# Kernel optimization log

Hardware: AMD Instinct MI355X
Metric: run time of the kernel (lower is better)

## Reference

```python
import jax, jax.numpy as jnp
import numpy as np

B, T, N = 8, 128, 64
K, d = 8, 64
D = K * d  # 512
NEG = -32767.0  # -2**15 + 1, as in the torch module


def _xavier(key, shape):
    fan_out, fan_in = shape
    limit = float(np.sqrt(6.0 / (fan_in + fan_out)))
    return jax.random.uniform(key, shape, jnp.float32, -limit, limit)


def setup_inputs() -> dict:
    key = jax.random.key(0)
    ks = jax.random.split(key, 6)
    X = jax.random.normal(ks[0], (B, T, N, D), jnp.float32)
    STE = jax.random.normal(ks[1], (B, T, N, 2 * D), jnp.float32)
    Wq = _xavier(ks[2], (D, 3 * D))
    Wk = _xavier(ks[3], (D, 3 * D))
    Wv = _xavier(ks[4], (D, 3 * D))
    Wo = _xavier(ks[5], (D, D))
    bq = jnp.zeros((D,), jnp.float32)
    bk = jnp.zeros((D,), jnp.float32)
    bv = jnp.zeros((D,), jnp.float32)
    bo = jnp.zeros((D,), jnp.float32)
    return {"X": X, "STE": STE, "Wq": Wq, "bq": bq, "Wk": Wk, "bk": bk,
            "Wv": Wv, "bv": bv, "Wo": Wo, "bo": bo}


def _fc(H, W, b):
    # 1x1 conv over channel dim == linear on last axis, then ReLU
    return jax.nn.relu(jnp.einsum('btnc,oc->btno', H, W) + b)


def _split_heads(x):
    # [B,T,N,D] -> [K,B,N,T,d]; torch splits last dim into K chunks of d and
    # stacks them along the batch dim (head-major), then permutes (0,2,1,3).
    return x.reshape(B, T, N, K, d).transpose(3, 0, 2, 1, 4)


def reference(X, STE, Wq, bq, Wk, bk, Wv, bv, Wo, bo):
    H = jnp.concatenate([X, STE], axis=-1)  # [B,T,N,3D]
    q = _split_heads(_fc(H, Wq, bq))  # [K,B,N,T,d]
    k = _split_heads(_fc(H, Wk, bk))
    v = _split_heads(_fc(H, Wv, bv))
    att = jnp.einsum('kbntd,kbnsd->kbnts', q, k) / jnp.sqrt(jnp.float32(d))
    causal = jnp.tril(jnp.ones((T, T), bool))  # [T,T]
    att = jnp.where(causal, att, NEG)
    att = jax.nn.softmax(att, axis=-1)
    out = jnp.einsum('kbnts,kbnsd->kbntd', att, v)  # [K,B,N,T,d]
    out = out.transpose(1, 3, 2, 0, 4).reshape(B, T, N, D)  # heads back to channels
    return jax.nn.relu(jnp.einsum('btnc,oc->btno', out, Wo) + bo)
```

## Files before the change

### kernel.cpp

```cpp
#include <hip/hip_runtime.h>
#include <hip/hip_bf16.h>


typedef __attribute__((ext_vector_type(8))) short short8;
typedef __attribute__((ext_vector_type(8))) _Float16 half8;
typedef __attribute__((ext_vector_type(4))) float floatx4;
typedef __attribute__((ext_vector_type(4))) unsigned int uintx4;

static __device__ __forceinline__ ushort f2b(float f) {
  __hip_bfloat16 h = __float2bfloat16(f);
  return __builtin_bit_cast(ushort, h);
}
static __device__ __forceinline__ ushort f2h(float f) {
  _Float16 h = (_Float16)f;
  return __builtin_bit_cast(ushort, h);
}
static __device__ __forceinline__ float blo(unsigned int w) {
  return __builtin_bit_cast(float, w << 16);
}
static __device__ __forceinline__ float bhi(unsigned int w) {
  return __builtin_bit_cast(float, w & 0xffff0000u);
}
static __device__ __forceinline__ uintx4 cvt8(const float* __restrict__ p) {
  const floatx4 f0 = *(const floatx4*)(p);
  const floatx4 f1 = *(const floatx4*)(p + 4);
  uintx4 r;
  r[0] = (unsigned int)f2b(f0[0]) | ((unsigned int)f2b(f0[1]) << 16);
  r[1] = (unsigned int)f2b(f0[2]) | ((unsigned int)f2b(f0[3]) << 16);
  r[2] = (unsigned int)f2b(f1[0]) | ((unsigned int)f2b(f1[1]) << 16);
  r[3] = (unsigned int)f2b(f1[2]) | ((unsigned int)f2b(f1[3]) << 16);
  return r;
}
static __device__ __forceinline__ void gld_lds16(const ushort* g, ushort* l) {
  __builtin_amdgcn_global_load_lds(
      (const __attribute__((address_space(1))) void*)g,
      (__attribute__((address_space(3))) void*)l, 16, 0, 0);
}

__global__ __launch_bounds__(256)
void cvt_bf16_pass(const float* __restrict__ X, const float* __restrict__ STE,
                   const float* __restrict__ Wq, const float* __restrict__ Wk,
                   const float* __restrict__ Wv, const float* __restrict__ Wo,
                   ushort* __restrict__ H, ushort* __restrict__ Wb,
                   ushort* __restrict__ Wob)
{
  const int stride = gridDim.x * blockDim.x;
  for (int c = blockIdx.x * blockDim.x + threadIdx.x; c < 12910592; c += stride) {
    const float* src; ushort* dst;
    if (c < 4194304) {
      const int m = c >> 6, col = (c & 63) << 3;
      src = X + ((size_t)c << 3);
      dst = H + (size_t)m * 1536 + col;
    } else if (c < 12582912) {
      const int c2 = c - 4194304;
      const int m = c2 >> 7, col = (c2 & 127) << 3;
      src = STE + ((size_t)c2 << 3);
      dst = H + (size_t)m * 1536 + 512 + col;
    } else if (c < 12877824) {
      const int c3 = c - 12582912;
      const int w = c3 / 98304;
      const int r = c3 - w * 98304;
      const float* Ws = (w == 0) ? Wq : (w == 1) ? Wk : Wv;
      src = Ws + ((size_t)r << 3);
      dst = Wb + ((size_t)c3 << 3);
    } else {
      const int c4 = c - 12877824;
      src = Wo + ((size_t)c4 << 3);
      dst = Wob + ((size_t)c4 << 3);
    }
    *(uintx4*)dst = cvt8(src);
  }
}

template<int KDIM, bool TRIPLE, bool OUT_F32>
__global__ __launch_bounds__(256, 2)
void gemm_bf16_async(const ushort* __restrict__ A, const ushort* __restrict__ Wall,
                     const float* __restrict__ b0, const float* __restrict__ b1,
                     const float* __restrict__ b2, void* __restrict__ Cv, int ldc)
{
  __shared__ ushort As[128 * 64];
  __shared__ ushort Bs[128 * 64];

  const int tn = blockIdx.x, tm = blockIdx.y;
  const int tid = threadIdx.x;
  const int wave = tid >> 6, lane = tid & 63;
  const int quad = lane >> 4, lid = lane & 15;
  const int wm = wave >> 1, wn = wave & 1;

  const ushort* W; const float* bias; int nbase, cbase;
  if (TRIPLE) {
    const int seg = tn >> 2;
    W = Wall + (size_t)seg * 512 * 1536;
    bias = (seg == 0) ? b0 : (seg == 1) ? b1 : b2;
    nbase = (tn & 3) * 128;
    cbase = seg * 512;
  } else { W = Wall; bias = b0; nbase = tn * 128; cbase = 0; }

  const int rloc = lane >> 3, sphys = lane & 7;

  floatx4 acc[4][4];
#pragma unroll
  for (int i = 0; i < 4; i++)
#pragma unroll
    for (int j = 0; j < 4; j++) acc[i][j] = (floatx4){0.f, 0.f, 0.f, 0.f};

  const char* AsB = (const char*)As;
  const char* BsB = (const char*)Bs;

  for (int kt = 0; kt < KDIM / 64; ++kt) {
#pragma unroll
    for (int i = 0; i < 4; i++) {
      const int row = (wave * 4 + i) * 8 + rloc;
      const int slog = sphys ^ (row & 7);
      const int k0 = kt * 64 + slog * 8;
      gld_lds16(A + (size_t)(tm * 128 + row) * KDIM + k0, As + (wave * 4 + i) * 512);
      gld_lds16(W + (size_t)(nbase + row) * KDIM + k0,    Bs + (wave * 4 + i) * 512);
    }
    __syncthreads();
#pragma unroll
    for (int ks = 0; ks < 2; ++ks) {
      short8 af[4], bfr[4];
#pragma unroll
      for (int t = 0; t < 4; t++) {
        const int ar = wm * 64 + t * 16 + lid;
        const int br = wn * 64 + t * 16 + lid;
        af[t]  = *(const short8*)(AsB + ar * 128 + (((ks * 4 + quad) ^ (ar & 7)) << 4));
        bfr[t] = *(const short8*)(BsB + br * 128 + (((ks * 4 + quad) ^ (br & 7)) << 4));
      }
#pragma unroll
      for (int i = 0; i < 4; i++)
#pragma unroll
        for (int j = 0; j < 4; j++)
          acc[i][j] = __builtin_amdgcn_mfma_f32_16x16x32_bf16(af[i], bfr[j], acc[i][j], 0, 0, 0);
    }
    __syncthreads();
  }

#pragma unroll
  for (int j = 0; j < 4; j++) {
    const int ncol = nbase + wn * 64 + j * 16 + lid;
    const float bv = bias[ncol];
    const int cg = cbase + ncol;
#pragma unroll
    for (int i = 0; i < 4; i++) {
      const int mrow = tm * 128 + wm * 64 + i * 16 + quad * 4;
#pragma unroll
      for (int r = 0; r < 4; r++) {
        float v = acc[i][j][r] + bv;
        v = v > 0.f ? v : 0.f;
        if (OUT_F32) ((float*)Cv)[(size_t)(mrow + r) * ldc + cg] = v;
        else         ((ushort*)Cv)[(size_t)(mrow + r) * ldc + cg] = f2b(v);
      }
    }
  }
}

__global__ __launch_bounds__(256, 2)
void attn_mfma(const ushort* __restrict__ qkv, ushort* __restrict__ outb)
{
  __shared__ ushort Ks[128 * 64];
  __shared__ ushort Vt[64 * 128];
  __shared__ ushort Ps[128 * 128];

  const int bx = blockIdx.x;
  const int head = bx >> 9;
  const int b = (bx >> 6) & 7;
  const int n = bx & 63;
  const int tid = threadIdx.x;
  const int wave = tid >> 6, lane = tid & 63;
  const int quad = lane >> 4, lid = lane & 15;

  char* KsB = (char*)Ks;
  char* VtB = (char*)Vt;
  char* PsB = (char*)Ps;

#pragma unroll
  for (int i = 0; i < 4; i++) {
    const int idx = tid + i * 256;
    const int s = idx >> 3, slot = idx & 7;
    const ushort* gb = qkv + ((size_t)((b * 128 + s) * 64 + n)) * 1536 + head * 64;
    const uintx4 kw = *(const uintx4*)(gb + 512 + slot * 8);
    *(uintx4*)(KsB + s * 128 + ((slot ^ (s & 7)) << 4)) = kw;
    const uintx4 vw = *(const uintx4*)(gb + 1024 + slot * 8);
#pragma unroll
    for (int j = 0; j < 4; j++) {
      const int d0 = slot * 8 + 2 * j;
      const int d1 = d0 + 1;
      *(ushort*)(VtB + d0 * 256 + (((s >> 3) ^ (d0 & 15)) << 4) + (s & 7) * 2) = f2h(blo(vw[j]));
      *(ushort*)(VtB + d1 * 256 + (((s >> 3) ^ (d1 & 15)) << 4) + (s & 7) * 2) = f2h(bhi(vw[j]));
    }
  }

  short8 qf[2][2];
#pragma unroll
  for (int i = 0; i < 2; i++)
#pragma unroll
    for (int ks = 0; ks < 2; ks++) {
      const int t = wave * 32 + i * 16 + lid;
      qf[i][ks] = *(const short8*)(qkv + ((size_t)((b * 128 + t) * 64 + n)) * 1536
                                   + head * 64 + ks * 32 + quad * 8);
    }
  __syncthreads();

  floatx4 acc[2][8];
#pragma unroll
  for (int i = 0; i < 2; i++)
#pragma unroll
    for (int j = 0; j < 8; j++) acc[i][j] = (floatx4){0.f, 0.f, 0.f, 0.f};

#pragma unroll
  for (int ks = 0; ks < 2; ks++) {
#pragma unroll
    for (int j = 0; j < 8; j++) {
      const int srow = j * 16 + lid;
      const short8 kf = *(const short8*)(KsB + srow * 128
                                         + (((ks * 4 + quad) ^ (srow & 7)) << 4));
#pragma unroll
      for (int i = 0; i < 2; i++)
        acc[i][j] = __builtin_amdgcn_mfma_f32_16x16x32_bf16(qf[i][ks], kf, acc[i][j], 0, 0, 0);
    }
  }

  float sum[2][4];
#pragma unroll
  for (int i = 0; i < 2; i++)
#pragma unroll
    for (int r = 0; r < 4; r++) {
      const int row = wave * 32 + i * 16 + quad * 4 + r;
      float m = -1e30f;
#pragma unroll
      for (int j = 0; j < 8; j++) {
        const int col = j * 16 + lid;
        float sv = acc[i][j][r] * 0.125f;
        sv = (col > row) ? -1e30f : sv;
        acc[i][j][r] = sv;
        m = fmaxf(m, sv);
      }
      m = fmaxf(m, __shfl_xor(m, 1));
      m = fmaxf(m, __shfl_xor(m, 2));
      m = fmaxf(m, __shfl_xor(m, 4));
      m = fmaxf(m, __shfl_xor(m, 8));
      float s = 0.f;
#pragma unroll
      for (int j = 0; j < 8; j++) {
        const float p = __expf(acc[i][j][r] - m);
        s += p;
        const int col = j * 16 + lid;
        *(ushort*)(PsB + row * 256 + (((col >> 3) ^ (row & 15)) << 4) + (col & 7) * 2) = f2h(p);
      }
      s += __shfl_xor(s, 1);
      s += __shfl_xor(s, 2);
      s += __shfl_xor(s, 4);
      s += __shfl_xor(s, 8);
      sum[i][r] = s;
    }
  __syncthreads();

  floatx4 acc2[2][4];
#pragma unroll
  for (int i = 0; i < 2; i++)
#pragma unroll
    for (int j2 = 0; j2 < 4; j2++) acc2[i][j2] = (floatx4){0.f, 0.f, 0.f, 0.f};

#pragma unroll
  for (int ks2 = 0; ks2 < 4; ks2++) {
    short8 pf[2];
#pragma unroll
    for (int i = 0; i < 2; i++) {
      const int row = wave * 32 + i * 16 + lid;
      pf[i] = *(const short8*)(PsB + row * 256 + (((ks2 * 4 + quad) ^ (row & 15)) << 4));
    }
#pragma unroll
    for (int j2 = 0; j2 < 4; j2++) {
      const int dd = j2 * 16 + lid;
      const short8 vf = *(const short8*)(VtB + dd * 256 + (((ks2 * 4 + quad) ^ (dd & 15)) << 4));
#pragma unroll
      for (int i = 0; i < 2; i++)
        acc2[i][j2] = __builtin_amdgcn_mfma_f32_16x16x32_f16(
            __builtin_bit_cast(half8, pf[i]), __builtin_bit_cast(half8, vf),
            acc2[i][j2], 0, 0, 0);
    }
  }

#pragma unroll
  for (int i = 0; i < 2; i++)
#pragma unroll
    for (int r = 0; r < 4; r++) {
      const float inv = 1.f / sum[i][r];
      const int t = wave * 32 + i * 16 + quad * 4 + r;
      ushort* ob = outb + ((size_t)((b * 128 + t) * 64 + n)) * 512 + head * 64;
#pragma unroll
      for (int j2 = 0; j2 < 4; j2++)
        ob[j2 * 16 + lid] = f2b(acc2[i][j2][r] * inv);
    }
}

extern "C" void kernel_launch(void* const* d_in, const int* in_sizes, int n_in,
                              void* d_out, int out_size, void* d_ws, size_t ws_size,
                              hipStream_t stream) {
  const float* X   = (const float*)d_in[0];
  const float* STE = (const float*)d_in[1];
  const float* Wq  = (const float*)d_in[2];
  const float* bq  = (const float*)d_in[3];
  const float* Wk  = (const float*)d_in[4];
  const float* bk  = (const float*)d_in[5];
  const float* Wv  = (const float*)d_in[6];
  const float* bv  = (const float*)d_in[7];
  const float* Wo  = (const float*)d_in[8];
  const float* bo  = (const float*)d_in[9];
  float* out = (float*)d_out;

  ushort* qkv = (ushort*)d_ws;
  ushort* H   = qkv + (size_t)65536 * 1536;
  ushort* att = H;
  ushort* Wb  = H + (size_t)65536 * 1536;
  ushort* Wob = Wb + (size_t)3 * 512 * 1536;

  cvt_bf16_pass<<<2048, 256, 0, stream>>>(X, STE, Wq, Wk, Wv, Wo, H, Wb, Wob);
  gemm_bf16_async<1536, true, false><<<dim3(12, 512), 256, 0, stream>>>(
      H, Wb, bq, bk, bv, qkv, 1536);
  attn_mfma<<<dim3(4096), 256, 0, stream>>>(qkv, att);
  gemm_bf16_async<512, false, true><<<dim3(4, 512), 256, 0, stream>>>(
      att, Wob, bo, nullptr, nullptr, out, 512);
}
```

Measured before the change: 970.0 us.

## Use 256x256 tiles with 8 waves and double-buffered LDS in GEMMs

The two projection GEMMs move from 128x128 tiles with 4 waves to 256x256 tiles with 8 waves. The K loop now double-buffers the LDS tiles, issuing the next tile's async global-to-LDS loads before computing on the current one and waiting with explicit vmcnt counts instead of two __syncthreads per step. MFMA sections get raised scheduling priority and sched barriers. This is meant to raise data reuse per tile and hide global load latency, at the cost of 128KB of LDS per block and more accumulator registers, which may limit occupancy.

```diff
diff --git a/kernel.cpp b/kernel.cpp
--- a/kernel.cpp
+++ b/kernel.cpp
@@ -73,80 +73,116 @@
 }
 
 template<int KDIM, bool TRIPLE, bool OUT_F32>
-__global__ __launch_bounds__(256, 2)
-void gemm_bf16_async(const ushort* __restrict__ A, const ushort* __restrict__ Wall,
-                     const float* __restrict__ b0, const float* __restrict__ b1,
-                     const float* __restrict__ b2, void* __restrict__ Cv, int ldc)
+__global__ __launch_bounds__(512, 2)
+void gemm_bf16_8p(const ushort* __restrict__ A, const ushort* __restrict__ Wall,
+                  const float* __restrict__ b0, const float* __restrict__ b1,
+                  const float* __restrict__ b2, void* __restrict__ Cv, int ldc)
 {
-  __shared__ ushort As[128 * 64];
-  __shared__ ushort Bs[128 * 64];
+  __shared__ ushort As[2][256 * 64];
+  __shared__ ushort Bs[2][256 * 64];
 
   const int tn = blockIdx.x, tm = blockIdx.y;
   const int tid = threadIdx.x;
   const int wave = tid >> 6, lane = tid & 63;
   const int quad = lane >> 4, lid = lane & 15;
-  const int wm = wave >> 1, wn = wave & 1;
+  const int wm = wave >> 2, wn = wave & 3;
 
   const ushort* W; const float* bias; int nbase, cbase;
   if (TRIPLE) {
-    const int seg = tn >> 2;
-    W = Wall + (size_t)seg * 512 * 1536;
+    const int seg = tn >> 1;
+    W = Wall + (size_t)seg * 512 * KDIM;
     bias = (seg == 0) ? b0 : (seg == 1) ? b1 : b2;
-    nbase = (tn & 3) * 128;
+    nbase = (tn & 1) * 256;
     cbase = seg * 512;
-  } else { W = Wall; bias = b0; nbase = tn * 128; cbase = 0; }
+  } else { W = Wall; bias = b0; nbase = tn * 256; cbase = 0; }
 
   const int rloc = lane >> 3, sphys = lane & 7;
-
-  floatx4 acc[4][4];
-#pragma unroll
-  for (int i = 0; i < 4; i++)
+  const ushort* ga[4]; const ushort* gb[4]; int ldso[4];
+#pragma unroll
+  for (int i = 0; i < 4; i++) {
+    const int row = i * 64 + wave * 8 + rloc;
+    const int slog = sphys ^ (row & 7);
+    ga[i] = A + (size_t)(tm * 256 + row) * KDIM + slog * 8;
+    gb[i] = W + (size_t)(nbase + row) * KDIM + slog * 8;
+    ldso[i] = (i * 512 + wave * 64) * 8;
+  }
+
+  constexpr int NT = KDIM / 64;
+
+#pragma unroll
+  for (int i = 0; i < 4; i++) {
+    gld_lds16(ga[i], &As[0][ldso[i]]);
+    gld_lds16(gb[i], &Bs[0][ldso[i]]);
+    ga[i] += 64; gb[i] += 64;
+  }
+
+  floatx4 acc[8][4];
+#pragma unroll
+  for (int i = 0; i < 8; i++)
 #pragma unroll
     for (int j = 0; j < 4; j++) acc[i][j] = (floatx4){0.f, 0.f, 0.f, 0.f};
 
-  const char* AsB = (const char*)As;
-  const char* BsB = (const char*)Bs;
-
-  for (int kt = 0; kt < KDIM / 64; ++kt) {
-#pragma unroll
-    for (int i = 0; i < 4; i++) {
-      const int row = (wave * 4 + i) * 8 + rloc;
-      const int slog = sphys ^ (row & 7);
-      const int k0 = kt * 64 + slog * 8;
-      gld_lds16(A + (size_t)(tm * 128 + row) * KDIM + k0, As + (wave * 4 + i) * 512);
-      gld_lds16(W + (size_t)(nbase + row) * KDIM + k0,    Bs + (wave * 4 + i) * 512);
-    }
-    __syncthreads();
+  int cur = 0;
+  for (int t = 0; t < NT; ++t) {
+    if (t + 1 < NT) {
+#pragma unroll
+      for (int i = 0; i < 4; i++) {
+        gld_lds16(ga[i], &As[cur ^ 1][ldso[i]]);
+        gld_lds16(gb[i], &Bs[cur ^ 1][ldso[i]]);
+        ga[i] += 64; gb[i] += 64;
+      }
+      asm volatile("s_waitcnt vmcnt(8)" ::: "memory");
+    } else {
+      asm volatile("s_waitcnt vmcnt(0)" ::: "memory");
+    }
+    __builtin_amdgcn_s_barrier();
+
+    const char* asB = (const char*)As[cur];
+    const char* bsB = (const char*)Bs[cur];
+    short8 bfr[4], af[4];
 #pragma unroll
     for (int ks = 0; ks < 2; ++ks) {
-      short8 af[4], bfr[4];
-#pragma unroll
-      for (int t = 0; t < 4; t++) {
-        const int ar = wm * 64 + t * 16 + lid;
-        const int br = wn * 64 + t * 16 + lid;
-        af[t]  = *(const short8*)(AsB + ar * 128 + (((ks * 4 + quad) ^ (ar & 7)) << 4));
-        bfr[t] = *(const short8*)(BsB + br * 128 + (((ks * 4 + quad) ^ (br & 7)) << 4));
-      }
-#pragma unroll
-      for (int i = 0; i < 4; i++)
-#pragma unroll
-        for (int j = 0; j < 4; j++)
-          acc[i][j] = __builtin_amdgcn_mfma_f32_16x16x32_bf16(af[i], bfr[j], acc[i][j], 0, 0, 0);
-    }
-    __syncthreads();
-  }
-
-#pragma unroll
-  for (int j = 0; j < 4; j++) {
-    const int ncol = nbase + wn * 64 + j * 16 + lid;
+#pragma unroll
+      for (int mh = 0; mh < 2; ++mh) {
+        if (mh == 0) {
+#pragma unroll
+          for (int n = 0; n < 4; n++) {
+            const int br = wn * 64 + n * 16 + lid;
+            bfr[n] = *(const short8*)(bsB + br * 128 + (((ks * 4 + quad) ^ (lid & 7)) << 4));
+          }
+        }
+#pragma unroll
+        for (int m = 0; m < 4; m++) {
+          const int ar = wm * 128 + (mh * 4 + m) * 16 + lid;
+          af[m] = *(const short8*)(asB + ar * 128 + (((ks * 4 + quad) ^ (lid & 7)) << 4));
+        }
+        asm volatile("s_waitcnt lgkmcnt(0)" ::: "memory");
+        __builtin_amdgcn_sched_barrier(0);
+        __builtin_amdgcn_s_setprio(1);
+#pragma unroll
+        for (int m = 0; m < 4; m++)
+#pragma unroll
+          for (int n = 0; n < 4; n++)
+            acc[mh * 4 + m][n] = __builtin_amdgcn_mfma_f32_16x16x32_bf16(
+                af[m], bfr[n], acc[mh * 4 + m][n], 0, 0, 0);
+        __builtin_amdgcn_s_setprio(0);
+        __builtin_amdgcn_s_barrier();
+      }
+    }
+    cur ^= 1;
+  }
+
+#pragma unroll
+  for (int n = 0; n < 4; n++) {
+    const int ncol = nbase + wn * 64 + n * 16 + lid;
     const float bv = bias[ncol];
     const int cg = cbase + ncol;
 #pragma unroll
-    for (int i = 0; i < 4; i++) {
-      const int mrow = tm * 128 + wm * 64 + i * 16 + quad * 4;
+    for (int mi = 0; mi < 8; mi++) {
+      const int mrow = tm * 256 + wm * 128 + mi * 16 + quad * 4;
 #pragma unroll
       for (int r = 0; r < 4; r++) {
-        float v = acc[i][j][r] + bv;
+        float v = acc[mi][n][r] + bv;
         v = v > 0.f ? v : 0.f;
         if (OUT_F32) ((float*)Cv)[(size_t)(mrow + r) * ldc + cg] = v;
         else         ((ushort*)Cv)[(size_t)(mrow + r) * ldc + cg] = f2b(v);
@@ -317,9 +353,9 @@
   ushort* Wob = Wb + (size_t)3 * 512 * 1536;
 
   cvt_bf16_pass<<<2048, 256, 0, stream>>>(X, STE, Wq, Wk, Wv, Wo, H, Wb, Wob);
-  gemm_bf16_async<1536, true, false><<<dim3(12, 512), 256, 0, stream>>>(
+  gemm_bf16_8p<1536, true, false><<<dim3(6, 256), 512, 0, stream>>>(
       H, Wb, bq, bk, bv, qkv, 1536);
   attn_mfma<<<dim3(4096), 256, 0, stream>>>(qkv, att);
-  gemm_bf16_async<512, false, true><<<dim3(4, 512), 256, 0, stream>>>(
+  gemm_bf16_8p<512, false, true><<<dim3(2, 256), 512, 0, stream>>>(
       att, Wob, bo, nullptr, nullptr, out, 512);
 }
```

Result: slower. 1.064 ms (+9.7%).

## Store QKV in head-major contiguous layout and split conversion pass by source

Applied to the files above, without the earlier changes.

The QKV projection GEMM epilogue now writes each (batch, node, head, q/k/v) slice as a contiguous 128x64 tile, so the attention kernel reads Q, K and V with unit-stride row loads instead of rows strided by 1536 elements. The bf16 conversion kernel gives each source tensor its own dedicated block range, removing the per-element branch chain. In exchange, the GEMM epilogue does scattered 2-byte stores with heavier index arithmetic per row, which may lower write coalescing.

```diff
diff --git a/kernel.cpp b/kernel.cpp
--- a/kernel.cpp
+++ b/kernel.cpp
@@ -44,35 +44,32 @@
                    ushort* __restrict__ H, ushort* __restrict__ Wb,
                    ushort* __restrict__ Wob)
 {
-  const int stride = gridDim.x * blockDim.x;
-  for (int c = blockIdx.x * blockDim.x + threadIdx.x; c < 12910592; c += stride) {
-    const float* src; ushort* dst;
-    if (c < 4194304) {
+  const int bid = blockIdx.x, tid = threadIdx.x;
+  if (bid < 1024) {
+    for (int c = bid * 256 + tid; c < 4194304; c += 1024 * 256) {
       const int m = c >> 6, col = (c & 63) << 3;
-      src = X + ((size_t)c << 3);
-      dst = H + (size_t)m * 1536 + col;
-    } else if (c < 12582912) {
-      const int c2 = c - 4194304;
-      const int m = c2 >> 7, col = (c2 & 127) << 3;
-      src = STE + ((size_t)c2 << 3);
-      dst = H + (size_t)m * 1536 + 512 + col;
-    } else if (c < 12877824) {
-      const int c3 = c - 12582912;
-      const int w = c3 / 98304;
-      const int r = c3 - w * 98304;
-      const float* Ws = (w == 0) ? Wq : (w == 1) ? Wk : Wv;
-      src = Ws + ((size_t)r << 3);
-      dst = Wb + ((size_t)c3 << 3);
-    } else {
-      const int c4 = c - 12877824;
-      src = Wo + ((size_t)c4 << 3);
-      dst = Wob + ((size_t)c4 << 3);
-    }
-    *(uintx4*)dst = cvt8(src);
-  }
-}
-
-template<int KDIM, bool TRIPLE, bool OUT_F32>
+      *(uintx4*)(H + (size_t)m * 1536 + col) = cvt8(X + ((size_t)c << 3));
+    }
+  } else if (bid < 2048) {
+    for (int c = (bid - 1024) * 256 + tid; c < 8388608; c += 1024 * 256) {
+      const int m = c >> 7, col = (c & 127) << 3;
+      *(uintx4*)(H + (size_t)m * 1536 + 512 + col) = cvt8(STE + ((size_t)c << 3));
+    }
+  } else {
+    for (int c = (bid - 2048) * 256 + tid; c < 327680; c += 128 * 256) {
+      if (c < 294912) {
+        const int w = c / 98304, r = c - w * 98304;
+        const float* Ws = (w == 0) ? Wq : (w == 1) ? Wk : Wv;
+        *(uintx4*)(Wb + ((size_t)c << 3)) = cvt8(Ws + ((size_t)r << 3));
+      } else {
+        const int c4 = c - 294912;
+        *(uintx4*)(Wob + ((size_t)c4 << 3)) = cvt8(Wo + ((size_t)c4 << 3));
+      }
+    }
+  }
+}
+
+template<int KDIM, bool TRIPLE, bool OUT_F32, bool QKV_OUT>
 __global__ __launch_bounds__(256, 2)
 void gemm_bf16_async(const ushort* __restrict__ A, const ushort* __restrict__ Wall,
                      const float* __restrict__ b0, const float* __restrict__ b1,
@@ -136,27 +133,50 @@
     __syncthreads();
   }
 
-#pragma unroll
-  for (int j = 0; j < 4; j++) {
-    const int ncol = nbase + wn * 64 + j * 16 + lid;
-    const float bv = bias[ncol];
-    const int cg = cbase + ncol;
+  float bvj[4];
+#pragma unroll
+  for (int j = 0; j < 4; j++) bvj[j] = bias[nbase + wn * 64 + j * 16 + lid];
+
+  if (QKV_OUT) {
+    const int head_w = (nbase + wn * 64) >> 6;
+    const int seg = cbase >> 9;
 #pragma unroll
     for (int i = 0; i < 4; i++) {
-      const int mrow = tm * 128 + wm * 64 + i * 16 + quad * 4;
 #pragma unroll
       for (int r = 0; r < 4; r++) {
-        float v = acc[i][j][r] + bv;
-        v = v > 0.f ? v : 0.f;
-        if (OUT_F32) ((float*)Cv)[(size_t)(mrow + r) * ldc + cg] = v;
-        else         ((ushort*)Cv)[(size_t)(mrow + r) * ldc + cg] = f2b(v);
+        const int m = tm * 128 + wm * 64 + i * 16 + quad * 4 + r;
+        const int b_ = m >> 13, t_ = (m >> 6) & 127, n_ = m & 63;
+        ushort* rowp = (ushort*)Cv
+            + ((((size_t)(b_ * 64 + n_) * 8 + head_w) * 3 + seg) << 13) + t_ * 64;
+#pragma unroll
+        for (int j = 0; j < 4; j++) {
+          float v = acc[i][j][r] + bvj[j];
+          v = v > 0.f ? v : 0.f;
+          rowp[j * 16 + lid] = f2b(v);
+        }
+      }
+    }
+  } else {
+#pragma unroll
+    for (int j = 0; j < 4; j++) {
+      const int cg = cbase + nbase + wn * 64 + j * 16 + lid;
+#pragma unroll
+      for (int i = 0; i < 4; i++) {
+        const int mrow = tm * 128 + wm * 64 + i * 16 + quad * 4;
+#pragma unroll
+        for (int r = 0; r < 4; r++) {
+          float v = acc[i][j][r] + bvj[j];
+          v = v > 0.f ? v : 0.f;
+          if (OUT_F32) ((float*)Cv)[(size_t)(mrow + r) * ldc + cg] = v;
+          else         ((ushort*)Cv)[(size_t)(mrow + r) * ldc + cg] = f2b(v);
+        }
       }
     }
   }
 }
 
 __global__ __launch_bounds__(256, 2)
-void attn_mfma(const ushort* __restrict__ qkv, ushort* __restrict__ outb)
+void attn_mfma(const ushort* __restrict__ qkv2, ushort* __restrict__ outb)
 {
   __shared__ ushort Ks[128 * 64];
   __shared__ ushort Vt[64 * 128];
@@ -174,14 +194,15 @@
   char* VtB = (char*)Vt;
   char* PsB = (char*)Ps;
 
+  const ushort* base = qkv2 + (((size_t)(b * 64 + n) * 8 + head) * 3 << 13);
+
 #pragma unroll
   for (int i = 0; i < 4; i++) {
     const int idx = tid + i * 256;
     const int s = idx >> 3, slot = idx & 7;
-    const ushort* gb = qkv + ((size_t)((b * 128 + s) * 64 + n)) * 1536 + head * 64;
-    const uintx4 kw = *(const uintx4*)(gb + 512 + slot * 8);
+    const uintx4 kw = *(const uintx4*)(base + 8192 + s * 64 + slot * 8);
     *(uintx4*)(KsB + s * 128 + ((slot ^ (s & 7)) << 4)) = kw;
-    const uintx4 vw = *(const uintx4*)(gb + 1024 + slot * 8);
+    const uintx4 vw = *(const uintx4*)(base + 16384 + s * 64 + slot * 8);
 #pragma unroll
     for (int j = 0; j < 4; j++) {
       const int d0 = slot * 8 + 2 * j;
@@ -197,8 +218,7 @@
 #pragma unroll
     for (int ks = 0; ks < 2; ks++) {
       const int t = wave * 32 + i * 16 + lid;
-      qf[i][ks] = *(const short8*)(qkv + ((size_t)((b * 128 + t) * 64 + n)) * 1536
-                                   + head * 64 + ks * 32 + quad * 8);
+      qf[i][ks] = *(const short8*)(base + t * 64 + ks * 32 + quad * 8);
     }
   __syncthreads();
 
@@ -310,16 +330,16 @@
   const float* bo  = (const float*)d_in[9];
   float* out = (float*)d_out;
 
-  ushort* qkv = (ushort*)d_ws;
-  ushort* H   = qkv + (size_t)65536 * 1536;
-  ushort* att = H;
+  ushort* qkv2 = (ushort*)d_ws;
+  ushort* H    = qkv2 + (size_t)65536 * 1536;
+  ushort* att  = H;
   ushort* Wb  = H + (size_t)65536 * 1536;
   ushort* Wob = Wb + (size_t)3 * 512 * 1536;
 
-  cvt_bf16_pass<<<2048, 256, 0, stream>>>(X, STE, Wq, Wk, Wv, Wo, H, Wb, Wob);
-  gemm_bf16_async<1536, true, false><<<dim3(12, 512), 256, 0, stream>>>(
-      H, Wb, bq, bk, bv, qkv, 1536);
-  attn_mfma<<<dim3(4096), 256, 0, stream>>>(qkv, att);
-  gemm_bf16_async<512, false, true><<<dim3(4, 512), 256, 0, stream>>>(
+  cvt_bf16_pass<<<2176, 256, 0, stream>>>(X, STE, Wq, Wk, Wv, Wo, H, Wb, Wob);
+  gemm_bf16_async<1536, true, false, true><<<dim3(12, 512), 256, 0, stream>>>(
+      H, Wb, bq, bk, bv, qkv2, 0);
+  attn_mfma<<<dim3(4096), 256, 0, stream>>>(qkv2, att);
+  gemm_bf16_async<512, false, true, false><<<dim3(4, 512), 256, 0, stream>>>(
       att, Wob, bo, nullptr, nullptr, out, 512);
 }
```

New measurement: 965.1 us. About the same (-0.5%).
